# Kernel optimization log

Hardware: AMD Instinct MI355X
Metric: run time of the kernel (lower is better)

The kernel has to match this reference:

```python
import jax, jax.numpy as jnp
import numpy as np

DIM = 1024
NUM_HEADS = 16
REL_DIM = 32
B, N = 8, 512


def setup_inputs() -> dict:
    key = jax.random.key(0)
    ks = jax.random.split(key, 8)
    s = 0.02
    return {
        "x": jax.random.normal(ks[0], (B, N, DIM), dtype=jnp.float32),
        "rel_bias": jax.random.normal(ks[1], (B, N, N, REL_DIM), dtype=jnp.float32),
        # torch nn.Linear convention: weight (out_features, in_features)
        "W_qkv": jax.random.normal(ks[2], (3 * DIM, DIM), dtype=jnp.float32) * s,
        "b_qkv": jax.random.normal(ks[3], (3 * DIM,), dtype=jnp.float32) * s,
        "W_rel": jax.random.normal(ks[4], (NUM_HEADS, REL_DIM), dtype=jnp.float32) * s,
        "b_rel": jax.random.normal(ks[5], (NUM_HEADS,), dtype=jnp.float32) * s,
        "W_out": jax.random.normal(ks[6], (DIM, DIM), dtype=jnp.float32) * s,
        "b_out": jax.random.normal(ks[7], (DIM,), dtype=jnp.float32) * s,
    }


def reference(x, rel_bias, W_qkv, b_qkv, W_rel, b_rel, W_out, b_out):
    Bx, Nx, D = x.shape
    H = NUM_HEADS
    hd = D // H
    # QKV projection: (B,N,3D) -> (B,N,3,H,hd)
    qkv = (x @ W_qkv.T + b_qkv).reshape(Bx, Nx, 3, H, hd)
    q, k, v = qkv[:, :, 0], qkv[:, :, 1], qkv[:, :, 2]
    scale = hd ** -0.5
    attn = jnp.einsum('bnhd,bmhd->bhnm', q, k) * scale
    # per-pair relative bias projected to heads: (B,N,N,H) -> (B,H,N,N)
    rel = (rel_bias @ W_rel.T + b_rel).transpose(0, 3, 1, 2)
    attn = jax.nn.softmax(attn + rel, axis=-1)
    out = jnp.einsum('bhnm,bmhd->bnhd', attn, v).reshape(Bx, Nx, D)
    return out @ W_out.T + b_out
```

## Files before the change

kernel.cpp:

```cpp
#include <hip/hip_runtime.h>

typedef unsigned short u16;
typedef unsigned int u32;
typedef __attribute__((ext_vector_type(8))) __bf16 bf16x8;
typedef __attribute__((ext_vector_type(4))) float f32x4;

union U8 {
  bf16x8 b;
  uint2 u2[2];
  uint4 u4;
  u32 w[4];
  u16 us[8];
};

__device__ __forceinline__ u16 f2bf(float f) {
  u32 x = __float_as_uint(f);
  x += 0x7FFFu + ((x >> 16) & 1u);
  return (u16)(x >> 16);
}
__device__ __forceinline__ float bf2f(u16 u) {
  return __uint_as_float(((u32)u) << 16);
}
__device__ __forceinline__ u32 cvtpk(float lo, float hi) {
  u32 r;
  asm("v_cvt_pk_bf16_f32 %0, %1, %2" : "=v"(r) : "v"(lo), "v"(hi));
  return r;
}

#define GLOAD16(gp, lp)                                                          \
  __builtin_amdgcn_global_load_lds(                                              \
      (const __attribute__((address_space(1))) unsigned int*)(const void*)(gp),  \
      (__attribute__((address_space(3))) unsigned int*)(void*)(lp), 16, 0, 0)

__global__ void k_convert_all(const float* __restrict__ x, const float* __restrict__ wq,
                              const float* __restrict__ wo, u16* __restrict__ xb,
                              u16* __restrict__ wqb, u16* __restrict__ wob) {
  const int NX = 1048576, NQ = 786432, NO = 262144;
  int idx = blockIdx.x * blockDim.x + threadIdx.x;
  int stride = gridDim.x * blockDim.x;
  for (int i = idx; i < NX + NQ + NO; i += stride) {
    const float4* s;
    ushort4* d;
    int k;
    if (i < NX) { s = (const float4*)x; d = (ushort4*)xb; k = i; }
    else if (i < NX + NQ) { s = (const float4*)wq; d = (ushort4*)wqb; k = i - NX; }
    else { s = (const float4*)wo; d = (ushort4*)wob; k = i - NX - NQ; }
    float4 v = s[k];
    ushort4 o;
    o.x = f2bf(v.x); o.y = f2bf(v.y); o.z = f2bf(v.z); o.w = f2bf(v.w);
    d[k] = o;
  }
}

__global__ __launch_bounds__(256) void k_rel(const float* __restrict__ rb,
                                             const float* __restrict__ Wr,
                                             const float* __restrict__ br,
                                             u16* __restrict__ out) {
  const int t = threadIdx.x;
  const int i16 = t & 15, j = (t >> 4) & 3, c = t >> 6;
  const int mt = blockIdx.x, ntg = blockIdx.y, b = blockIdx.z;
  const int nt = ntg >> 2, g = ntg & 3;
  const int n = nt * 16 + 4 * g + j;
  const int m = mt * 64 + c * 16 + i16;

  const float4* rp = (const float4*)(rb + ((size_t)(b * 512 + n) * 512 + m) * 32);
  float4 r4[8];
#pragma unroll
  for (int q = 0; q < 8; ++q) r4[q] = rp[q];

  const size_t obase =
      (((size_t)(b * 16) * 32 + nt) * 8 + mt) * 1024 + c * 256 + (g * 16 + i16) * 4 + j;
#pragma unroll
  for (int h = 0; h < 16; ++h) {
    float acc = br[h];
    const float* w = Wr + h * 32;
#pragma unroll
    for (int q = 0; q < 8; ++q) {
      acc += r4[q].x * w[4 * q + 0] + r4[q].y * w[4 * q + 1] +
             r4[q].z * w[4 * q + 2] + r4[q].w * w[4 * q + 3];
    }
    out[obase + (size_t)h * 262144] = f2bf(acc);
  }
}

__global__ __launch_bounds__(256) void k_gemm_qkv(const u16* __restrict__ A,
                                                  const u16* __restrict__ Bm,
                                                  const float* __restrict__ bias,
                                                  u16* __restrict__ Qo, u16* __restrict__ Ko,
                                                  u16* __restrict__ Vo) {
  const int K = 1024;
  __shared__ u16 Al[128 * 64];
  __shared__ u16 Bl[128 * 64];
  const int t = threadIdx.x;
  const int lane = t & 63, wid = t >> 6;
  const int g = lane >> 4, i16 = lane & 15;
  const int wm = wid >> 1, wn = wid & 1;
  const int bm = blockIdx.y, bn = blockIdx.x;

  f32x4 zero = {0.f, 0.f, 0.f, 0.f};
  f32x4 acc[4][4];
#pragma unroll
  for (int mi = 0; mi < 4; ++mi)
#pragma unroll
    for (int ni = 0; ni < 4; ++ni) acc[mi][ni] = zero;

  int srow[4], sgc[4];
#pragma unroll
  for (int i = 0; i < 4; ++i) {
    int ch = wid * 256 + i * 64 + lane;
    int r = ch >> 3, cs = ch & 7;
    srow[i] = r;
    sgc[i] = cs ^ (r & 7);
  }

  for (int k0 = 0; k0 < K; k0 += 64) {
    __syncthreads();
#pragma unroll
    for (int i = 0; i < 4; ++i) {
      const u16* ga = A + (size_t)(bm * 128 + srow[i]) * K + k0 + sgc[i] * 8;
      const u16* gb = Bm + (size_t)(bn * 128 + srow[i]) * K + k0 + sgc[i] * 8;
      GLOAD16(ga, Al + (size_t)(wid * 256 + i * 64) * 8);
      GLOAD16(gb, Bl + (size_t)(wid * 256 + i * 64) * 8);
    }
    __syncthreads();

#pragma unroll
    for (int kk = 0; kk < 2; ++kk) {
      U8 af[4], bfr[4];
#pragma unroll
      for (int mi = 0; mi < 4; ++mi) {
        int row = wm * 64 + mi * 16 + i16;
        int ch = (g + 4 * kk) ^ (row & 7);
        af[mi].u4 = *(const uint4*)(Al + row * 64 + ch * 8);
      }
#pragma unroll
      for (int ni = 0; ni < 4; ++ni) {
        int row = wn * 64 + ni * 16 + i16;
        int ch = (g + 4 * kk) ^ (row & 7);
        bfr[ni].u4 = *(const uint4*)(Bl + row * 64 + ch * 8);
      }
#pragma unroll
      for (int mi = 0; mi < 4; ++mi)
#pragma unroll
        for (int ni = 0; ni < 4; ++ni)
          acc[mi][ni] = __builtin_amdgcn_mfma_f32_16x16x32_bf16(af[mi].b, bfr[ni].b,
                                                                acc[mi][ni], 0, 0, 0);
    }
  }

#pragma unroll
  for (int mi = 0; mi < 4; ++mi) {
#pragma unroll
    for (int ni = 0; ni < 4; ++ni) {
      int col = bn * 128 + wn * 64 + ni * 16 + i16;
      int row0 = bm * 128 + wm * 64 + mi * 16 + 4 * g;
      float bia = bias[col];
      int tt = col >> 10;
      int h = (col >> 6) & 15;
      int d = col & 63;
      int b = row0 >> 9;
      int n0 = row0 & 511;
      if (tt < 2) {
        u16* dst = (tt == 0) ? Qo : Ko;
#pragma unroll
        for (int j = 0; j < 4; ++j)
          dst[((size_t)(b * 16 + h) * 512 + n0 + j) * 64 + d] = f2bf(acc[mi][ni][j] + bia);
      } else {
        uint2 w;
        w.x = cvtpk(acc[mi][ni][0] + bia, acc[mi][ni][1] + bia);
        w.y = cvtpk(acc[mi][ni][2] + bia, acc[mi][ni][3] + bia);
        *(uint2*)(Vo + ((size_t)(b * 16 + h) * 64 + d) * 512 + n0) = w;
      }
    }
  }
}

__global__ __launch_bounds__(256) void k_gemm_out(const u16* __restrict__ A,
                                                  const u16* __restrict__ Bm,
                                                  const float* __restrict__ bias,
                                                  float* __restrict__ Co) {
  const int K = 1024;
  __shared__ u16 Al[128 * 64];
  __shared__ u16 Bl[128 * 64];
  const int t = threadIdx.x;
  const int lane = t & 63, wid = t >> 6;
  const int g = lane >> 4, i16 = lane & 15;
  const int wm = wid >> 1, wn = wid & 1;
  const int bm = blockIdx.y, bn = blockIdx.x;

  f32x4 zero = {0.f, 0.f, 0.f, 0.f};
  f32x4 acc[4][4];
#pragma unroll
  for (int mi = 0; mi < 4; ++mi)
#pragma unroll
    for (int ni = 0; ni < 4; ++ni) acc[mi][ni] = zero;

  int srow[4], sgc[4];
#pragma unroll
  for (int i = 0; i < 4; ++i) {
    int ch = wid * 256 + i * 64 + lane;
    int r = ch >> 3, cs = ch & 7;
    srow[i] = r;
    sgc[i] = cs ^ (r & 7);
  }

  for (int k0 = 0; k0 < K; k0 += 64) {
    __syncthreads();
#pragma unroll
    for (int i = 0; i < 4; ++i) {
      GLOAD16(A + (size_t)(bm * 128 + srow[i]) * K + k0 + sgc[i] * 8,
              Al + (size_t)(wid * 256 + i * 64) * 8);
      GLOAD16(Bm + (size_t)(bn * 128 + srow[i]) * K + k0 + sgc[i] * 8,
              Bl + (size_t)(wid * 256 + i * 64) * 8);
    }
    __syncthreads();

#pragma unroll
    for (int kk = 0; kk < 2; ++kk) {
      U8 af[4], bfr[4];
#pragma unroll
      for (int mi = 0; mi < 4; ++mi) {
        int row = wm * 64 + mi * 16 + i16;
        int ch = (g + 4 * kk) ^ (row & 7);
        af[mi].u4 = *(const uint4*)(Al + row * 64 + ch * 8);
      }
#pragma unroll
      for (int ni = 0; ni < 4; ++ni) {
        int row = wn * 64 + ni * 16 + i16;
        int ch = (g + 4 * kk) ^ (row & 7);
        bfr[ni].u4 = *(const uint4*)(Bl + row * 64 + ch * 8);
      }
#pragma unroll
      for (int mi = 0; mi < 4; ++mi)
#pragma unroll
        for (int ni = 0; ni < 4; ++ni)
          acc[mi][ni] = __builtin_amdgcn_mfma_f32_16x16x32_bf16(af[mi].b, bfr[ni].b,
                                                                acc[mi][ni], 0, 0, 0);
    }
  }

#pragma unroll
  for (int mi = 0; mi < 4; ++mi) {
#pragma unroll
    for (int ni = 0; ni < 4; ++ni) {
      int col = bn * 128 + wn * 64 + ni * 16 + i16;
      int row0 = bm * 128 + wm * 64 + mi * 16 + 4 * g;
      float bia = bias[col];
#pragma unroll
      for (int j = 0; j < 4; ++j)
        Co[(size_t)(row0 + j) * 1024 + col] = acc[mi][ni][j] + bia;
    }
  }
}

__global__ __launch_bounds__(256) void k_attn(const u16* __restrict__ Q,
                                              const u16* __restrict__ Kb,
                                              const u16* __restrict__ Vtb,
                                              const u16* __restrict__ Rel,
                                              u16* __restrict__ Out) {
  __shared__ u16 Kl[2][64 * 64];
  __shared__ u16 Vl[2][64 * 64];
  __shared__ u16 Pl[4][16 * 68];

  const int qt = blockIdx.x, h = blockIdx.y, b = blockIdx.z;
  const int t = threadIdx.x, lane = t & 63, wid = t >> 6;
  const int g = lane >> 4, i16 = lane & 15;
  const size_t bh = (size_t)(b * 16 + h);

  const u16* Qg = Q + (bh * 512 + qt * 64 + wid * 16 + i16) * 64;
  U8 qf[2];
  qf[0].u4 = *(const uint4*)(Qg + 8 * g);
  qf[1].u4 = *(const uint4*)(Qg + 8 * g + 32);

  float m_run[4], l_run[4];
  f32x4 zero = {0.f, 0.f, 0.f, 0.f};
  f32x4 acc[4];
#pragma unroll
  for (int c = 0; c < 4; ++c) acc[c] = zero;
#pragma unroll
  for (int j = 0; j < 4; ++j) { m_run[j] = -1e30f; l_run[j] = 0.f; }

  int srow[2], sgc[2];
#pragma unroll
  for (int i = 0; i < 2; ++i) {
    int ch = wid * 128 + i * 64 + lane;
    int r = ch >> 3, cs = ch & 7;
    srow[i] = r;
    sgc[i] = cs ^ (r & 7);
  }

  const u16* Kg0 = Kb + bh * 512 * 64;
  const u16* Vg0 = Vtb + bh * 64 * 512;
  const u16* Rg = Rel + ((bh * 32 + qt * 4 + wid) * 8) * 1024 + lane * 4;

#define STAGE(buf, m0)                                                                  \
  do {                                                                                  \
    _Pragma("unroll") for (int i = 0; i < 2; ++i) {                                     \
      GLOAD16(Kg0 + (size_t)((m0) + srow[i]) * 64 + sgc[i] * 8,                         \
              &Kl[buf][(size_t)(wid * 128 + i * 64) * 8]);                              \
      GLOAD16(Vg0 + (size_t)srow[i] * 512 + (m0) + sgc[i] * 8,                          \
              &Vl[buf][(size_t)(wid * 128 + i * 64) * 8]);                              \
    }                                                                                   \
  } while (0)

  STAGE(0, 0);
  __syncthreads();

  for (int it = 0; it < 8; ++it) {
    const int buf = it & 1;
    if (it < 7) STAGE(buf ^ 1, it * 64 + 64);

    uint2 rl[4];
#pragma unroll
    for (int c = 0; c < 4; ++c) rl[c] = *(const uint2*)(Rg + it * 1024 + c * 256);

    f32x4 s[4];
#pragma unroll
    for (int c = 0; c < 4; ++c) s[c] = zero;
    __builtin_amdgcn_s_setprio(1);
#pragma unroll
    for (int c = 0; c < 4; ++c) {
#pragma unroll
      for (int kk = 0; kk < 2; ++kk) {
        int row = c * 16 + i16;
        int ch = (g + 4 * kk) ^ (row & 7);
        U8 kf;
        kf.u4 = *(const uint4*)(&Kl[buf][row * 64 + ch * 8]);
        s[c] = __builtin_amdgcn_mfma_f32_16x16x32_bf16(qf[kk].b, kf.b, s[c], 0, 0, 0);
      }
    }
    __builtin_amdgcn_s_setprio(0);

#pragma unroll
    for (int c = 0; c < 4; ++c) {
      const u16* rc = (const u16*)&rl[c];
#pragma unroll
      for (int j = 0; j < 4; ++j) s[c][j] = s[c][j] * 0.125f + bf2f(rc[j]);
    }
    float fac[4];
#pragma unroll
    for (int j = 0; j < 4; ++j) {
      float pm = fmaxf(fmaxf(s[0][j], s[1][j]), fmaxf(s[2][j], s[3][j]));
      pm = fmaxf(pm, __shfl_xor(pm, 1));
      pm = fmaxf(pm, __shfl_xor(pm, 2));
      pm = fmaxf(pm, __shfl_xor(pm, 4));
      pm = fmaxf(pm, __shfl_xor(pm, 8));
      float mnew = fmaxf(m_run[j], pm);
      fac[j] = __expf(m_run[j] - mnew);
      m_run[j] = mnew;
    }
#pragma unroll
    for (int c = 0; c < 4; ++c)
#pragma unroll
      for (int j = 0; j < 4; ++j) s[c][j] = __expf(s[c][j] - m_run[j]);
#pragma unroll
    for (int j = 0; j < 4; ++j) {
      float rs = s[0][j] + s[1][j] + s[2][j] + s[3][j];
      rs += __shfl_xor(rs, 1);
      rs += __shfl_xor(rs, 2);
      rs += __shfl_xor(rs, 4);
      rs += __shfl_xor(rs, 8);
      l_run[j] = l_run[j] * fac[j] + rs;
    }
#pragma unroll
    for (int c = 0; c < 4; ++c)
#pragma unroll
      for (int j = 0; j < 4; ++j) acc[c][j] *= fac[j];

    u16* Pw = Pl[wid];
#pragma unroll
    for (int c = 0; c < 4; ++c)
#pragma unroll
      for (int j = 0; j < 4; ++j)
        Pw[(4 * g + j) * 68 + c * 16 + i16] = f2bf(s[c][j]);

    U8 pf[2];
#pragma unroll
    for (int kk = 0; kk < 2; ++kk) {
      const u16* p = Pl[wid] + i16 * 68 + 8 * g + 32 * kk;
      pf[kk].u2[0] = *(const uint2*)p;
      pf[kk].u2[1] = *(const uint2*)(p + 4);
    }
    __builtin_amdgcn_s_setprio(1);
#pragma unroll
    for (int c = 0; c < 4; ++c) {
#pragma unroll
      for (int kk = 0; kk < 2; ++kk) {
        int row = c * 16 + i16;
        int ch = (g + 4 * kk) ^ (row & 7);
        U8 vf;
        vf.u4 = *(const uint4*)(&Vl[buf][row * 64 + ch * 8]);
        acc[c] = __builtin_amdgcn_mfma_f32_16x16x32_bf16(pf[kk].b, vf.b, acc[c], 0, 0, 0);
      }
    }
    __builtin_amdgcn_s_setprio(0);
    __syncthreads();
  }
#undef STAGE

#pragma unroll
  for (int c = 0; c < 4; ++c) {
#pragma unroll
    for (int j = 0; j < 4; ++j) {
      int n = qt * 64 + wid * 16 + 4 * g + j;
      float v = acc[c][j] / l_run[j];
      Out[((size_t)b * 512 + n) * 1024 + h * 64 + c * 16 + i16] = f2bf(v);
    }
  }
}

extern "C" void kernel_launch(void* const* d_in, const int* in_sizes, int n_in,
                              void* d_out, int out_size, void* d_ws, size_t ws_size,
                              hipStream_t stream) {
  const float* x = (const float*)d_in[0];
  const float* rel_bias = (const float*)d_in[1];
  const float* W_qkv = (const float*)d_in[2];
  const float* b_qkv = (const float*)d_in[3];
  const float* W_rel = (const float*)d_in[4];
  const float* b_rel = (const float*)d_in[5];
  const float* W_out = (const float*)d_in[6];
  const float* b_out = (const float*)d_in[7];
  float* out = (float*)d_out;

  char* ws = (char*)d_ws;
  u16* x_bf    = (u16*)(ws);
  u16* wqkv_bf = (u16*)(ws + 8388608);
  u16* wout_bf = (u16*)(ws + 14680064);
  u16* Qw      = (u16*)(ws + 16777216);
  u16* Kw      = (u16*)(ws + 25165824);
  u16* Vt      = (u16*)(ws + 33554432);
  u16* relb    = (u16*)(ws + 41943040);
  u16* attno   = (u16*)(ws + 109051904);

  k_convert_all<<<2048, 256, 0, stream>>>(x, W_qkv, W_out, x_bf, wqkv_bf, wout_bf);

  k_rel<<<dim3(8, 128, 8), 256, 0, stream>>>(rel_bias, W_rel, b_rel, relb);

  k_gemm_qkv<<<dim3(24, 32), 256, 0, stream>>>(x_bf, wqkv_bf, b_qkv, Qw, Kw, Vt);

  k_attn<<<dim3(8, 16, 8), 256, 0, stream>>>(Qw, Kw, Vt, relb, attno);

  k_gemm_out<<<dim3(8, 32), 256, 0, stream>>>(attno, wout_bf, b_out, out);
}
```

Measured before the change: 191.0 us.

## Fuse relative-bias projection into attention kernel, one block per query tile covering all heads

```diff
diff --git a/kernel.cpp b/kernel.cpp
--- a/kernel.cpp
+++ b/kernel.cpp
@@ -52,37 +52,6 @@
   }
 }
 
-__global__ __launch_bounds__(256) void k_rel(const float* __restrict__ rb,
-                                             const float* __restrict__ Wr,
-                                             const float* __restrict__ br,
-                                             u16* __restrict__ out) {
-  const int t = threadIdx.x;
-  const int i16 = t & 15, j = (t >> 4) & 3, c = t >> 6;
-  const int mt = blockIdx.x, ntg = blockIdx.y, b = blockIdx.z;
-  const int nt = ntg >> 2, g = ntg & 3;
-  const int n = nt * 16 + 4 * g + j;
-  const int m = mt * 64 + c * 16 + i16;
-
-  const float4* rp = (const float4*)(rb + ((size_t)(b * 512 + n) * 512 + m) * 32);
-  float4 r4[8];
-#pragma unroll
-  for (int q = 0; q < 8; ++q) r4[q] = rp[q];
-
-  const size_t obase =
-      (((size_t)(b * 16) * 32 + nt) * 8 + mt) * 1024 + c * 256 + (g * 16 + i16) * 4 + j;
-#pragma unroll
-  for (int h = 0; h < 16; ++h) {
-    float acc = br[h];
-    const float* w = Wr + h * 32;
-#pragma unroll
-    for (int q = 0; q < 8; ++q) {
-      acc += r4[q].x * w[4 * q + 0] + r4[q].y * w[4 * q + 1] +
-             r4[q].z * w[4 * q + 2] + r4[q].w * w[4 * q + 3];
-    }
-    out[obase + (size_t)h * 262144] = f2bf(acc);
-  }
-}
-
 __global__ __launch_bounds__(256) void k_gemm_qkv(const u16* __restrict__ A,
                                                   const u16* __restrict__ Bm,
                                                   const float* __restrict__ bias,
@@ -253,21 +222,42 @@
   }
 }
 
-__global__ __launch_bounds__(256) void k_attn(const u16* __restrict__ Q,
-                                              const u16* __restrict__ Kb,
-                                              const u16* __restrict__ Vtb,
-                                              const u16* __restrict__ Rel,
-                                              u16* __restrict__ Out) {
-  __shared__ u16 Kl[2][64 * 64];
-  __shared__ u16 Vl[2][64 * 64];
-  __shared__ u16 Pl[4][16 * 68];
-
-  const int qt = blockIdx.x, h = blockIdx.y, b = blockIdx.z;
-  const int t = threadIdx.x, lane = t & 63, wid = t >> 6;
+__global__ __launch_bounds__(1024) void k_attn_rel(
+    const u16* __restrict__ Q, const u16* __restrict__ Kb, const u16* __restrict__ Vtb,
+    const float* __restrict__ rb, const float* __restrict__ Wr, const float* __restrict__ br,
+    u16* __restrict__ Out) {
+  __shared__ u16 relP[2][16 * 1024];
+  __shared__ u16 Pl[16][16 * 68];
+
+  const int nt = blockIdx.x, b = blockIdx.y;
+  const int t = threadIdx.x;
+  const int lane = t & 63, wid = t >> 6;
   const int g = lane >> 4, i16 = lane & 15;
-  const size_t bh = (size_t)(b * 16 + h);
-
-  const u16* Qg = Q + (bh * 512 + qt * 64 + wid * 16 + i16) * 64;
+  const size_t bh = (size_t)(b * 16 + wid);
+
+  const int pr_i16 = t & 15, pr_j = (t >> 4) & 3, pr_gg = (t >> 6) & 3, pr_c = t >> 8;
+  const int pr_n = nt * 16 + 4 * pr_gg + pr_j;
+  const int pr_moff = pr_c * 16 + pr_i16;
+  const float* pr_base = rb + ((size_t)(b * 512 + pr_n) * 512 + pr_moff) * 32;
+  const int pr_sto = pr_c * 256 + (pr_gg * 16 + pr_i16) * 4 + pr_j;
+
+#define REL_A(bufi, iti)                                                              \
+  do {                                                                                \
+    const float4* rp = (const float4*)(pr_base + (size_t)(iti) * 2048);               \
+    float4 r4[8];                                                                     \
+    _Pragma("unroll") for (int q = 0; q < 8; ++q) r4[q] = rp[q];                      \
+    _Pragma("unroll") for (int h = 0; h < 16; ++h) {                                  \
+      float a = br[h];                                                                \
+      const float* w = Wr + h * 32;                                                   \
+      _Pragma("unroll") for (int q = 0; q < 8; ++q) {                                 \
+        a += r4[q].x * w[4 * q] + r4[q].y * w[4 * q + 1] + r4[q].z * w[4 * q + 2] +   \
+             r4[q].w * w[4 * q + 3];                                                  \
+      }                                                                               \
+      relP[bufi][h * 1024 + pr_sto] = f2bf(a);                                        \
+    }                                                                                 \
+  } while (0)
+
+  const u16* Qg = Q + (bh * 512 + nt * 16 + i16) * 64;
   U8 qf[2];
   qf[0].u4 = *(const uint4*)(Qg + 8 * g);
   qf[1].u4 = *(const uint4*)(Qg + 8 * g + 32);
@@ -280,63 +270,45 @@
 #pragma unroll
   for (int j = 0; j < 4; ++j) { m_run[j] = -1e30f; l_run[j] = 0.f; }
 
-  int srow[2], sgc[2];
-#pragma unroll
-  for (int i = 0; i < 2; ++i) {
-    int ch = wid * 128 + i * 64 + lane;
-    int r = ch >> 3, cs = ch & 7;
-    srow[i] = r;
-    sgc[i] = cs ^ (r & 7);
-  }
-
-  const u16* Kg0 = Kb + bh * 512 * 64;
-  const u16* Vg0 = Vtb + bh * 64 * 512;
-  const u16* Rg = Rel + ((bh * 32 + qt * 4 + wid) * 8) * 1024 + lane * 4;
-
-#define STAGE(buf, m0)                                                                  \
-  do {                                                                                  \
-    _Pragma("unroll") for (int i = 0; i < 2; ++i) {                                     \
-      GLOAD16(Kg0 + (size_t)((m0) + srow[i]) * 64 + sgc[i] * 8,                         \
-              &Kl[buf][(size_t)(wid * 128 + i * 64) * 8]);                              \
-      GLOAD16(Vg0 + (size_t)srow[i] * 512 + (m0) + sgc[i] * 8,                          \
-              &Vl[buf][(size_t)(wid * 128 + i * 64) * 8]);                              \
-    }                                                                                   \
-  } while (0)
-
-  STAGE(0, 0);
+  const u16* Kg0 = Kb + bh * 32768;
+  const u16* Vg0 = Vtb + bh * 32768;
+
+  REL_A(0, 0);
   __syncthreads();
 
   for (int it = 0; it < 8; ++it) {
     const int buf = it & 1;
-    if (it < 7) STAGE(buf ^ 1, it * 64 + 64);
-
-    uint2 rl[4];
-#pragma unroll
-    for (int c = 0; c < 4; ++c) rl[c] = *(const uint2*)(Rg + it * 1024 + c * 256);
+    const int m0 = it * 64;
+
+    if (it < 7) REL_A(buf ^ 1, it + 1);
+
+    U8 tile[4][2];
+#pragma unroll
+    for (int c = 0; c < 4; ++c)
+#pragma unroll
+      for (int kk = 0; kk < 2; ++kk)
+        tile[c][kk].u4 =
+            *(const uint4*)(Kg0 + (size_t)(m0 + c * 16 + i16) * 64 + 8 * g + 32 * kk);
 
     f32x4 s[4];
 #pragma unroll
     for (int c = 0; c < 4; ++c) s[c] = zero;
     __builtin_amdgcn_s_setprio(1);
 #pragma unroll
+    for (int c = 0; c < 4; ++c)
+#pragma unroll
+      for (int kk = 0; kk < 2; ++kk)
+        s[c] = __builtin_amdgcn_mfma_f32_16x16x32_bf16(qf[kk].b, tile[c][kk].b, s[c], 0, 0, 0);
+    __builtin_amdgcn_s_setprio(0);
+
+#pragma unroll
     for (int c = 0; c < 4; ++c) {
-#pragma unroll
-      for (int kk = 0; kk < 2; ++kk) {
-        int row = c * 16 + i16;
-        int ch = (g + 4 * kk) ^ (row & 7);
-        U8 kf;
-        kf.u4 = *(const uint4*)(&Kl[buf][row * 64 + ch * 8]);
-        s[c] = __builtin_amdgcn_mfma_f32_16x16x32_bf16(qf[kk].b, kf.b, s[c], 0, 0, 0);
-      }
-    }
-    __builtin_amdgcn_s_setprio(0);
-
-#pragma unroll
-    for (int c = 0; c < 4; ++c) {
-      const u16* rc = (const u16*)&rl[c];
+      uint2 rr = *(const uint2*)(&relP[buf][wid * 1024 + c * 256 + lane * 4]);
+      const u16* rc = (const u16*)&rr;
 #pragma unroll
       for (int j = 0; j < 4; ++j) s[c][j] = s[c][j] * 0.125f + bf2f(rc[j]);
     }
+
     float fac[4];
 #pragma unroll
     for (int j = 0; j < 4; ++j) {
@@ -381,30 +353,33 @@
       pf[kk].u2[0] = *(const uint2*)p;
       pf[kk].u2[1] = *(const uint2*)(p + 4);
     }
+
+#pragma unroll
+    for (int c = 0; c < 4; ++c)
+#pragma unroll
+      for (int kk = 0; kk < 2; ++kk)
+        tile[c][kk].u4 =
+            *(const uint4*)(Vg0 + (size_t)(c * 16 + i16) * 512 + m0 + 8 * g + 32 * kk);
+
     __builtin_amdgcn_s_setprio(1);
 #pragma unroll
-    for (int c = 0; c < 4; ++c) {
-#pragma unroll
-      for (int kk = 0; kk < 2; ++kk) {
-        int row = c * 16 + i16;
-        int ch = (g + 4 * kk) ^ (row & 7);
-        U8 vf;
-        vf.u4 = *(const uint4*)(&Vl[buf][row * 64 + ch * 8]);
-        acc[c] = __builtin_amdgcn_mfma_f32_16x16x32_bf16(pf[kk].b, vf.b, acc[c], 0, 0, 0);
-      }
-    }
+    for (int c = 0; c < 4; ++c)
+#pragma unroll
+      for (int kk = 0; kk < 2; ++kk)
+        acc[c] = __builtin_amdgcn_mfma_f32_16x16x32_bf16(pf[kk].b, tile[c][kk].b, acc[c], 0, 0, 0);
     __builtin_amdgcn_s_setprio(0);
+
     __syncthreads();
   }
-#undef STAGE
+#undef REL_A
 
 #pragma unroll
   for (int c = 0; c < 4; ++c) {
 #pragma unroll
     for (int j = 0; j < 4; ++j) {
-      int n = qt * 64 + wid * 16 + 4 * g + j;
+      int n = nt * 16 + 4 * g + j;
       float v = acc[c][j] / l_run[j];
-      Out[((size_t)b * 512 + n) * 1024 + h * 64 + c * 16 + i16] = f2bf(v);
+      Out[((size_t)b * 512 + n) * 1024 + wid * 64 + c * 16 + i16] = f2bf(v);
     }
   }
 }
@@ -429,16 +404,13 @@
   u16* Qw      = (u16*)(ws + 16777216);
   u16* Kw      = (u16*)(ws + 25165824);
   u16* Vt      = (u16*)(ws + 33554432);
-  u16* relb    = (u16*)(ws + 41943040);
   u16* attno   = (u16*)(ws + 109051904);
 
   k_convert_all<<<2048, 256, 0, stream>>>(x, W_qkv, W_out, x_bf, wqkv_bf, wout_bf);
 
-  k_rel<<<dim3(8, 128, 8), 256, 0, stream>>>(rel_bias, W_rel, b_rel, relb);
-
   k_gemm_qkv<<<dim3(24, 32), 256, 0, stream>>>(x_bf, wqkv_bf, b_qkv, Qw, Kw, Vt);
 
-  k_attn<<<dim3(8, 16, 8), 256, 0, stream>>>(Qw, Kw, Vt, relb, attno);
+  k_attn_rel<<<dim3(32, 8), 1024, 0, stream>>>(Qw, Kw, Vt, rel_bias, W_rel, b_rel, attno);
 
   k_gemm_out<<<dim3(8, 32), 256, 0, stream>>>(attno, wout_bf, b_out, out);
 }
```

Measured after the change: 209.6 us. 9.7% more time.
